# Optimization experiments

Measured on AMD Instinct MI355X. Metric: run time of the kernel, lower is better.

## Reference

```python
import jax, jax.numpy as jnp
import numpy as np
from jax import lax


def _lstm_last(x, Wih, Whh, bih, bhh):
    """Single-layer torch-style LSTM (gate order i,f,g,o); returns last hidden state.
    x: (M, T, F) -> (M, H)."""
    gx = jnp.einsum('mtf,gf->mtg', x, Wih) + bih + bhh  # precompute input contributions
    H = Whh.shape[1]
    Wh = Whh.T
    def step(carry, g):
        h, c = carry
        z = g + h @ Wh
        i, f, gg, o = jnp.split(z, 4, axis=-1)
        c = jax.nn.sigmoid(f) * c + jax.nn.sigmoid(i) * jnp.tanh(gg)
        h = jax.nn.sigmoid(o) * jnp.tanh(c)
        return (h, c), None
    M = x.shape[0]
    init = (jnp.zeros((M, H), x.dtype), jnp.zeros((M, H), x.dtype))
    (h, _), _ = lax.scan(step, init, jnp.swapaxes(gx, 0, 1))
    return h


def _forward(input_data, rel_encoding, lstm_Wih, lstm_Whh, lstm_bih, lstm_bhh,
             hop_w1, hop_b1, hop_w2, hop_b2, fn_w1, fn_b1, fn_w2, fn_b2):
    B, W, N, F = input_data.shape
    U = lstm_Whh.shape[1]
    # SequentialEmbedding: per-stock LSTM over the window, take last step
    x = jnp.transpose(input_data, (0, 2, 1, 3)).reshape(B * N, W, F)
    seq = _lstm_last(x, lstm_Wih, lstm_Whh, lstm_bih, lstm_bhh).reshape(B, N, U)

    # RelationalEmbedding: dense N x N k-hop message passing
    mask = (rel_encoding.sum(-1) > 0).astype(seq.dtype)  # (N,N)
    D = mask.sum(-1)                                      # (N,) degrees (self-loops keep >0)
    e = seq
    for k in range(hop_w1.shape[0]):  # k_hops: small fixed loop
        W1 = hop_w1[k]
        # mask * concat([e_i, e_j, enc]) @ W1 + b1, computed blockwise without
        # materializing the (B,N,N,2U+K) concat; mask scales only the pre-bias term
        xi = e @ W1[:U]                                    # (B,N,INP)
        xj = e @ W1[U:2 * U]                               # (B,N,INP)
        xe = jnp.einsum('ijk,kp->ijp', rel_encoding, W1[2 * U:])  # (N,N,INP)
        pre = mask[None, :, :, None] * (xi[:, :, None, :] + xj[:, None, :, :] + xe[None]) + hop_b1[k]
        hdn = jax.nn.leaky_relu(pre)                       # (B,N,N,INP)
        wts = jax.nn.leaky_relu(hdn @ hop_w2[k] + hop_b2[k])[..., 0]  # (B,N,N)
        scaled = (wts * mask) / D[None, :, None]
        # torch: sum_i scaled[b,i,j] * e_j  ==  e_j * (sum_i scaled[b,i,j])
        e = scaled.sum(axis=1)[..., None] * e

    # FullyConnected head: Linear(2U,2U)+LeakyReLU, Linear(2U,1)+LeakyReLU, squeeze
    comb = jnp.concatenate([seq, e], axis=-1)              # (B,N,2U)
    out = jax.nn.leaky_relu(comb @ fn_w1 + fn_b1)
    out = jax.nn.leaky_relu(out @ fn_w2 + fn_b2)
    return out[..., 0]                                     # (B,N)


def setup_inputs() -> dict:
    key = jax.random.key(0)
    ks = jax.random.split(key, 14)
    B, W, N, F = 2, 32, 768, 4
    U, K, KH = 32, 8, 2
    INP = 2 * U + K  # 72
    def w(k, shape, fan):
        return jax.random.normal(k, shape, jnp.float32) / np.float32(np.sqrt(fan))
    enc = (jax.random.uniform(ks[1], (N, N, K)) < 0.05).astype(jnp.float32)
    # self-loops in relation channel 0 so every node has degree >= 1
    enc = enc.at[:, :, 0].set(jnp.maximum(enc[:, :, 0], jnp.eye(N, dtype=jnp.float32)))
    return {
        'input_data': jax.random.normal(ks[0], (B, W, N, F), jnp.float32),
        'rel_encoding': enc,
        'lstm_Wih': w(ks[2], (4 * U, F), F),
        'lstm_Whh': w(ks[3], (4 * U, U), U),
        'lstm_bih': 0.01 * jax.random.normal(ks[4], (4 * U,), jnp.float32),
        'lstm_bhh': 0.01 * jax.random.normal(ks[5], (4 * U,), jnp.float32),
        'hop_w1': w(ks[6], (KH, INP, INP), INP),
        'hop_b1': 0.01 * jax.random.normal(ks[7], (KH, INP), jnp.float32),
        'hop_w2': w(ks[8], (KH, INP, 1), INP),
        'hop_b2': 0.01 * jax.random.normal(ks[9], (KH, 1), jnp.float32),
        'fn_w1': w(ks[10], (2 * U, 2 * U), 2 * U),
        'fn_b1': 0.01 * jax.random.normal(ks[11], (2 * U,), jnp.float32),
        'fn_w2': w(ks[12], (2 * U, 1), 2 * U),
        'fn_b2': 0.01 * jax.random.normal(ks[13], (1,), jnp.float32),
    }


def reference(input_data, rel_encoding, lstm_Wih, lstm_Whh, lstm_bih, lstm_bhh,
              hop_w1, hop_b1, hop_w2, hop_b2, fn_w1, fn_b1, fn_w2, fn_b2):
    return _forward(input_data, rel_encoding, lstm_Wih, lstm_Whh, lstm_bih, lstm_bhh,
                    hop_w1, hop_b1, hop_w2, hop_b2, fn_w1, fn_b1, fn_w2, fn_b2)
```

## Files before the change

kernel.cpp:

```cpp
#include <hip/hip_runtime.h>

#define N_STK 768
#define BATCH 2
#define WIN   32
#define FEAT  4
#define UNITS 32
#define INP   72
#define LROW  76
#define NSLC  19
#define IPH   48
#define JCR   24
#define NPHI  16
#define NCR   32

__device__ __forceinline__ float lrelu(float v){ return v > 0.0f ? v : 0.01f*v; }
__device__ __forceinline__ float lanebcast(float v, int l){
    return __int_as_float(__builtin_amdgcn_readlane(__float_as_int(v), l));
}
__device__ __forceinline__ unsigned patof(const float* __restrict__ p){
    float4 a = *reinterpret_cast<const float4*>(p);
    float4 b = *reinterpret_cast<const float4*>(p + 4);
    unsigned m = 0;
    m |= (a.x != 0.0f) ? 1u   : 0u;
    m |= (a.y != 0.0f) ? 2u   : 0u;
    m |= (a.z != 0.0f) ? 4u   : 0u;
    m |= (a.w != 0.0f) ? 8u   : 0u;
    m |= (b.x != 0.0f) ? 16u  : 0u;
    m |= (b.y != 0.0f) ? 32u  : 0u;
    m |= (b.z != 0.0f) ? 64u  : 0u;
    m |= (b.w != 0.0f) ? 128u : 0u;
    return m;
}
__device__ __forceinline__ void async_cp16(const float* g, float* l){
    __builtin_amdgcn_global_load_lds(
        (const __attribute__((address_space(1))) unsigned int*)g,
        (__attribute__((address_space(3))) unsigned int*)l,
        16, 0, 0);
}

__global__ __launch_bounds__(256) void k1_kernel(const float* __restrict__ rel,
        const float* __restrict__ x, const float* __restrict__ Wih,
        const float* __restrict__ Whh, const float* __restrict__ bih,
        const float* __restrict__ bhh, const float* __restrict__ hop_w1,
        const float* __restrict__ hop_b1,
        float* __restrict__ seq, float* __restrict__ invD,
        unsigned char* __restrict__ Pout,
        float* __restrict__ lutlo, float* __restrict__ luthi,
        float* __restrict__ xi0, float* __restrict__ xj0,
        float* __restrict__ s0, float* __restrict__ s1){
    int j = blockIdx.x, tid = threadIdx.x;
    int wv = tid >> 6, lane = tid & 63;
    __shared__ float hrow[2][UNITS];
    __shared__ int cw_sh[2];

    if (wv < 2){
        int b = wv;
        int r0 = lane, r1 = 64 + lane;
        bool low = (lane < 32);
        float4 wi0 = *reinterpret_cast<const float4*>(Wih + r0*FEAT);
        float4 wi1 = *reinterpret_cast<const float4*>(Wih + r1*FEAT);
        float bb0 = bih[r0] + bhh[r0];
        float bb1 = bih[r1] + bhh[r1];
        float4 W0[8], W1[8];
        #pragma unroll
        for (int q = 0; q < 8; q++){
            W0[q] = *reinterpret_cast<const float4*>(Whh + r0*UNITS + q*4);
            W1[q] = *reinterpret_cast<const float4*>(Whh + r1*UNITS + q*4);
        }
        float4 xv = make_float4(0.f, 0.f, 0.f, 0.f);
        if (low) xv = *reinterpret_cast<const float4*>(x + ((size_t)(b*WIN + lane)*N_STK + j)*FEAT);
        float hreg = 0.0f, c = 0.0f;
        #pragma unroll 1
        for (int t = 0; t < WIN; t++){
            float xb0 = lanebcast(xv.x, t), xb1 = lanebcast(xv.y, t);
            float xb2 = lanebcast(xv.z, t), xb3 = lanebcast(xv.w, t);
            float z0a = bb0 + wi0.x*xb0 + wi0.z*xb2;
            float z0b =       wi0.y*xb1 + wi0.w*xb3;
            float z1a = bb1 + wi1.x*xb0 + wi1.z*xb2;
            float z1b =       wi1.y*xb1 + wi1.w*xb3;
            #pragma unroll
            for (int q = 0; q < 8; q++){
                float h0 = lanebcast(hreg, 32 + q*4 + 0);
                float h1 = lanebcast(hreg, 32 + q*4 + 1);
                float h2 = lanebcast(hreg, 32 + q*4 + 2);
                float h3 = lanebcast(hreg, 32 + q*4 + 3);
                z0a += W0[q].x*h0; z0b += W0[q].y*h1;
                z0a += W0[q].z*h2; z0b += W0[q].w*h3;
                z1a += W1[q].x*h0; z1b += W1[q].y*h1;
                z1a += W1[q].z*h2; z1b += W1[q].w*h3;
            }
            float z0 = z0a + z0b, z1 = z1a + z1b;
            float e0 = __expf(-z0);
            float sg = 1.0f/(1.0f + e0);
            float sc = low ? -2.0f : -1.0f;
            float e1 = __expf(sc*z1);
            float rr = 1.0f/(1.0f + e1);
            float act = low ? (1.0f - e1)*rr : rr;
            float pa = sg*act;
            float po = __shfl_xor(pa, 32);
            c = sg*c + po;
            float e2 = __expf(-2.0f*c);
            float th = (1.0f - e2)/(1.0f + e2);
            hreg = act*th;
        }
        if (!low){
            hrow[b][lane - 32] = hreg;
            seq[((size_t)b*N_STK + j)*UNITS + (lane - 32)] = hreg;
        }
    } else {
        int half = wv - 2;
        int local = 0;
        #pragma unroll
        for (int k = 0; k < 6; k++){
            int col = half*384 + k*64 + lane;
            unsigned pt = patof(rel + ((size_t)j*N_STK + col)*8);
            Pout[(size_t)j*N_STK + col] = (unsigned char)pt;
            local += pt ? 1 : 0;
        }
        #pragma unroll
        for (int d = 32; d; d >>= 1) local += __shfl_xor(local, d);
        if (lane == 0) cw_sh[half] = local;
    }
    __syncthreads();
    if (tid == 0){
        invD[j] = 1.0f/(float)(cw_sh[0] + cw_sh[1]);
        s0[j] = 0.0f; s0[N_STK + j] = 0.0f;
        s1[j] = 0.0f; s1[N_STK + j] = 0.0f;
    }
    if (j < 64 && tid >= 144 && tid < 216){
        int pp = tid - 144;
        int m = j & 15, half = (j >> 4) & 1, k = j >> 5;
        const float* W = hop_w1 + (size_t)k*INP*INP;
        float acc = half ? 0.0f : hop_b1[k*INP + pp];
        int base = 2*UNITS + (half ? 4 : 0);
        #pragma unroll
        for (int q = 0; q < 4; q++)
            if ((m >> q) & 1) acc += W[(base + q)*INP + pp];
        (half ? luthi : lutlo)[(k*16 + m)*INP + pp] = acc;
    }
    if (tid < 2*INP){
        int b = tid/INP, pp = tid - b*INP;
        float si = 0.0f, sj = 0.0f;
        #pragma unroll
        for (int u = 0; u < UNITS; u++){
            float ev = hrow[b][u];
            si += ev * hop_w1[u*INP + pp];
            sj += ev * hop_w1[(UNITS + u)*INP + pp];
        }
        size_t o = ((size_t)b*N_STK + j)*INP + pp;
        xi0[o] = si; xj0[o] = sj;
    }
}

__global__ __launch_bounds__(256) void hop_kernel(const float* __restrict__ xi,
        const float* __restrict__ xj,
        const float* __restrict__ lutlo_k, const float* __restrict__ luthi_k,
        const float* __restrict__ w2, const float* __restrict__ b2,
        const unsigned char* __restrict__ P, const float* __restrict__ invD,
        float* __restrict__ s_out){
    int cr = blockIdx.x, ip = blockIdx.y, b = blockIdx.z;
    int j0 = cr*JCR, i0 = ip*IPH, tid = threadIdx.x;
    __shared__ float xi_sh[IPH*LROW];
    __shared__ float xj_sh[JCR*LROW];
    __shared__ float lo_sh[16*LROW];
    __shared__ float hi_sh[16*LROW];
    __shared__ float invD_sh[IPH];
    __shared__ float acc_sh[JCR];
    __shared__ unsigned elist[IPH*JCR];
    __shared__ int n0_sh, nt_sh;

    const float* xib = xi + ((size_t)b*N_STK + i0)*INP;
    const float* xjb = xj + ((size_t)b*N_STK + j0)*INP;
    if (tid >= 224 && tid < 224 + JCR) acc_sh[tid - 224] = 0.0f;

    for (int u = tid; u < IPH*NSLC; u += 256){
        int r = u/NSLC, sl = u - r*NSLC;
        int off = (sl < 18) ? sl*4 : 0;
        async_cp16(xib + (size_t)r*INP + off, &xi_sh[0] + (size_t)u*4);
    }
    for (int u = tid; u < JCR*NSLC; u += 256){
        int r = u/NSLC, sl = u - r*NSLC;
        int off = (sl < 18) ? sl*4 : 0;
        async_cp16(xjb + (size_t)r*INP + off, &xj_sh[0] + (size_t)u*4);
    }
    for (int u = tid; u < 16*NSLC; u += 256){
        int r = u/NSLC, sl = u - r*NSLC;
        int off = (sl < 18) ? sl*4 : 0;
        async_cp16(lutlo_k + r*INP + off, &lo_sh[0] + (size_t)u*4);
    }
    for (int u = tid; u < 16*NSLC; u += 256){
        int r = u/NSLC, sl = u - r*NSLC;
        int off = (sl < 18) ? sl*4 : 0;
        async_cp16(luthi_k + r*INP + off, &hi_sh[0] + (size_t)u*4);
    }
    if (tid < IPH/4) async_cp16(invD + i0 + tid*4, &invD_sh[0] + tid*4);

    if (tid < 64){
        unsigned w[6] = {0,0,0,0,0,0};
        int c0 = 0, c1 = 0;
        if (tid < IPH){
            const unsigned* prow = reinterpret_cast<const unsigned*>(P + (size_t)(i0 + tid)*N_STK + j0);
            #pragma unroll
            for (int k = 0; k < 6; k++) w[k] = prow[k];
            #pragma unroll
            for (int k = 0; k < 24; k++){
                unsigned pat = (w[k >> 2] >> ((k & 3)*8)) & 255u;
                c0 += (pat && pat < 16u) ? 1 : 0;
                c1 += (pat >= 16u) ? 1 : 0;
            }
        }
        int s0v = c0, s1v = c1;
        #pragma unroll
        for (int off = 1; off < 64; off <<= 1){
            int a0 = __shfl_up(s0v, off), a1 = __shfl_up(s1v, off);
            if (tid >= off){ s0v += a0; s1v += a1; }
        }
        int N0 = __shfl(s0v, 63);
        int Nt = N0 + __shfl(s1v, 63);
        if (tid < IPH){
            int p0 = s0v - c0, p1 = N0 + s1v - c1;
            #pragma unroll
            for (int k = 0; k < 24; k++){
                unsigned pat = (w[k >> 2] >> ((k & 3)*8)) & 255u;
                unsigned enc = ((unsigned)tid << 13) | ((unsigned)k << 8) | pat;
                if (pat && pat < 16u) elist[p0++] = enc;
                else if (pat >= 16u)  elist[p1++] = enc;
            }
        }
        if (tid == 0){ n0_sh = N0; nt_sh = Nt; }
    }

    int hf = tid & 1;
    float4 w2r[9];
    #pragma unroll
    for (int q = 0; q < 9; q++) w2r[q] = *reinterpret_cast<const float4*>(w2 + hf*36 + q*4);
    float b2v = b2[0];
    __syncthreads();

    int n0 = n0_sh, ntot = nt_sh;
    for (int sl = tid >> 1; sl < n0; sl += 128){
        unsigned ent = elist[sl];
        int il = ent >> 13, jl = (ent >> 8) & 31, mlo = (int)(ent & 15u);
        const float* xr = &xi_sh[il*LROW + hf*36];
        const float* jr = &xj_sh[jl*LROW + hf*36];
        const float* lr = &lo_sh[mlo*LROW + hf*36];
        float dot = 0.0f;
        #pragma unroll
        for (int q = 0; q < 9; q++){
            float4 xv = *reinterpret_cast<const float4*>(xr + q*4);
            float4 jv = *reinterpret_cast<const float4*>(jr + q*4);
            float4 lv = *reinterpret_cast<const float4*>(lr + q*4);
            float4 w  = w2r[q];
            dot += lrelu(xv.x + jv.x + lv.x)*w.x;
            dot += lrelu(xv.y + jv.y + lv.y)*w.y;
            dot += lrelu(xv.z + jv.z + lv.z)*w.z;
            dot += lrelu(xv.w + jv.w + lv.w)*w.w;
        }
        dot += __shfl_xor(dot, 1);
        if (hf == 0) atomicAdd(&acc_sh[jl], lrelu(dot + b2v)*invD_sh[il]);
    }
    for (int sl = n0 + (tid >> 1); sl < ntot; sl += 128){
        unsigned ent = elist[sl];
        int il = ent >> 13, jl = (ent >> 8) & 31;
        int mlo = (int)(ent & 15u), mhi = (int)((ent >> 4) & 15u);
        const float* xr = &xi_sh[il*LROW + hf*36];
        const float* jr = &xj_sh[jl*LROW + hf*36];
        const float* lr = &lo_sh[mlo*LROW + hf*36];
        const float* hr = &hi_sh[mhi*LROW + hf*36];
        float dot = 0.0f;
        #pragma unroll
        for (int q = 0; q < 9; q++){
            float4 xv = *reinterpret_cast<const float4*>(xr + q*4);
            float4 jv = *reinterpret_cast<const float4*>(jr + q*4);
            float4 lv = *reinterpret_cast<const float4*>(lr + q*4);
            float4 hv = *reinterpret_cast<const float4*>(hr + q*4);
            float4 w  = w2r[q];
            dot += lrelu(xv.x + jv.x + lv.x + hv.x)*w.x;
            dot += lrelu(xv.y + jv.y + lv.y + hv.y)*w.y;
            dot += lrelu(xv.z + jv.z + lv.z + hv.z)*w.z;
            dot += lrelu(xv.w + jv.w + lv.w + hv.w)*w.w;
        }
        dot += __shfl_xor(dot, 1);
        if (hf == 0) atomicAdd(&acc_sh[jl], lrelu(dot + b2v)*invD_sh[il]);
    }
    __syncthreads();
    if (tid < JCR) atomicAdd(&s_out[b*N_STK + j0 + tid], acc_sh[tid]);
}

template<int MODE>
__global__ __launch_bounds__(192) void ep_kernel(const float* __restrict__ s0v,
        const float* __restrict__ s1v, const float* __restrict__ seqg,
        const float* __restrict__ W1next, float* __restrict__ xi_next,
        float* __restrict__ xj_next,
        const float* __restrict__ fw1, const float* __restrict__ fb1,
        const float* __restrict__ fw2, const float* __restrict__ fb2,
        float* __restrict__ outp){
    int j = blockIdx.x, tid = threadIdx.x;
    __shared__ float e_sh[2][64];
    if (tid < 64){
        int b = tid >> 5, u = tid & 31;
        size_t o = ((size_t)b*N_STK + j)*UNITS + u;
        float sv = seqg[o];
        if (MODE == 0){
            e_sh[b][u] = sv*s0v[b*N_STK + j];
        } else {
            e_sh[b][u] = sv;
            e_sh[b][32 + u] = sv*s0v[b*N_STK + j]*s1v[b*N_STK + j];
        }
    }
    __syncthreads();
    if (MODE == 0){
        if (tid < 2*INP){
            int b = tid/INP, pp = tid - b*INP;
            float si = 0.0f, sj = 0.0f;
            #pragma unroll
            for (int u = 0; u < UNITS; u++){
                float ev = e_sh[b][u];
                si += ev * W1next[u*INP + pp];
                sj += ev * W1next[(UNITS + u)*INP + pp];
            }
            size_t o = ((size_t)b*N_STK + j)*INP + pp;
            xi_next[o] = si; xj_next[o] = sj;
        }
    } else {
        if (tid < 128){
            int b = tid >> 6, u = tid & 63;
            float acc = fb1[u];
            #pragma unroll 8
            for (int d = 0; d < 64; d++) acc += e_sh[b][d]*fw1[d*64 + u];
            float prod = lrelu(acc)*fw2[u];
            prod += __shfl_xor(prod, 32);
            prod += __shfl_xor(prod, 16);
            prod += __shfl_xor(prod, 8);
            prod += __shfl_xor(prod, 4);
            prod += __shfl_xor(prod, 2);
            prod += __shfl_xor(prod, 1);
            if (u == 0) outp[b*N_STK + j] = lrelu(prod + fb2[0]);
        }
    }
}

extern "C" void kernel_launch(void* const* d_in, const int* in_sizes, int n_in,
                              void* d_out, int out_size, void* d_ws, size_t ws_size,
                              hipStream_t stream){
    const float* input_data = (const float*)d_in[0];
    const float* rel        = (const float*)d_in[1];
    const float* lstm_Wih   = (const float*)d_in[2];
    const float* lstm_Whh   = (const float*)d_in[3];
    const float* lstm_bih   = (const float*)d_in[4];
    const float* lstm_bhh   = (const float*)d_in[5];
    const float* hop_w1     = (const float*)d_in[6];
    const float* hop_b1     = (const float*)d_in[7];
    const float* hop_w2     = (const float*)d_in[8];
    const float* hop_b2     = (const float*)d_in[9];
    const float* fn_w1      = (const float*)d_in[10];
    const float* fn_b1      = (const float*)d_in[11];
    const float* fn_w2      = (const float*)d_in[12];
    const float* fn_b2      = (const float*)d_in[13];
    float* out = (float*)d_out;

    float* ws    = (float*)d_ws;
    float* seq   = ws;
    float* xi0   = seq   + 49152;
    float* xj0   = xi0   + 110592;
    float* xi1   = xj0   + 110592;
    float* xj1   = xi1   + 110592;
    float* lutlo = xj1   + 110592;
    float* luthi = lutlo + 2304;
    float* invD  = luthi + 2304;
    float* s0    = invD  + 768;
    float* s1    = s0    + 1536;
    unsigned char* P = (unsigned char*)(s1 + 1536);

    k1_kernel<<<N_STK, 256, 0, stream>>>(rel, input_data, lstm_Wih, lstm_Whh,
            lstm_bih, lstm_bhh, hop_w1, hop_b1,
            seq, invD, P, lutlo, luthi, xi0, xj0, s0, s1);

    dim3 hgrid(NCR, NPHI, BATCH);
    hop_kernel<<<hgrid, 256, 0, stream>>>(xi0, xj0, lutlo, luthi,
            hop_w2, hop_b2, P, invD, s0);

    ep_kernel<0><<<N_STK, 192, 0, stream>>>(s0, nullptr, seq,
            hop_w1 + INP*INP, xi1, xj1,
            nullptr, nullptr, nullptr, nullptr, nullptr);

    hop_kernel<<<hgrid, 256, 0, stream>>>(xi1, xj1, lutlo + 16*INP, luthi + 16*INP,
            hop_w2 + INP, hop_b2 + 1, P, invD, s1);

    ep_kernel<1><<<N_STK, 192, 0, stream>>>(s0, s1, seq,
            nullptr, nullptr, nullptr,
            fn_w1, fn_b1, fn_w2, fn_b2, out);
}
```

Measured before the change: 149.1 us.

## Precompute second-hop projections in LSTM kernel and scale by s0 inside hop kernel

Because e after the first hop equals seq scaled by a per-node scalar, the second hop's xi/xj projections are linear in that scalar. k1 now also computes seq@W1[hop1] projections, and the second hop kernel multiplies them by s0[i] and s0[j] on the fly. This removes the intermediate ep_kernel launch and its global round-trip. The cost is extra multiplies in the hop inner loop and more work in k1.

```diff
diff --git a/kernel.cpp b/kernel.cpp
--- a/kernel.cpp
+++ b/kernel.cpp
@@ -47,6 +47,7 @@
         unsigned char* __restrict__ Pout,
         float* __restrict__ lutlo, float* __restrict__ luthi,
         float* __restrict__ xi0, float* __restrict__ xj0,
+        float* __restrict__ yi1, float* __restrict__ yj1,
         float* __restrict__ s0, float* __restrict__ s1){
     int j = blockIdx.x, tid = threadIdx.x;
     int wv = tid >> 6, lane = tid & 63;
@@ -140,24 +141,30 @@
     }
     if (tid < 2*INP){
         int b = tid/INP, pp = tid - b*INP;
-        float si = 0.0f, sj = 0.0f;
+        const float* Wa = hop_w1;
+        const float* Wb = hop_w1 + INP*INP;
+        float si0 = 0.0f, sj0 = 0.0f, si1 = 0.0f, sj1 = 0.0f;
         #pragma unroll
         for (int u = 0; u < UNITS; u++){
             float ev = hrow[b][u];
-            si += ev * hop_w1[u*INP + pp];
-            sj += ev * hop_w1[(UNITS + u)*INP + pp];
+            si0 += ev * Wa[u*INP + pp];
+            sj0 += ev * Wa[(UNITS + u)*INP + pp];
+            si1 += ev * Wb[u*INP + pp];
+            sj1 += ev * Wb[(UNITS + u)*INP + pp];
         }
         size_t o = ((size_t)b*N_STK + j)*INP + pp;
-        xi0[o] = si; xj0[o] = sj;
-    }
-}
-
+        xi0[o] = si0; xj0[o] = sj0;
+        yi1[o] = si1; yj1[o] = sj1;
+    }
+}
+
+template<int SCALED>
 __global__ __launch_bounds__(256) void hop_kernel(const float* __restrict__ xi,
         const float* __restrict__ xj,
         const float* __restrict__ lutlo_k, const float* __restrict__ luthi_k,
         const float* __restrict__ w2, const float* __restrict__ b2,
         const unsigned char* __restrict__ P, const float* __restrict__ invD,
-        float* __restrict__ s_out){
+        const float* __restrict__ sscale, float* __restrict__ s_out){
     int cr = blockIdx.x, ip = blockIdx.y, b = blockIdx.z;
     int j0 = cr*JCR, i0 = ip*IPH, tid = threadIdx.x;
     __shared__ float xi_sh[IPH*LROW];
@@ -165,6 +172,8 @@
     __shared__ float lo_sh[16*LROW];
     __shared__ float hi_sh[16*LROW];
     __shared__ float invD_sh[IPH];
+    __shared__ float sI_sh[IPH];
+    __shared__ float sJ_sh[JCR];
     __shared__ float acc_sh[JCR];
     __shared__ unsigned elist[IPH*JCR];
     __shared__ int n0_sh, nt_sh;
@@ -172,6 +181,11 @@
     const float* xib = xi + ((size_t)b*N_STK + i0)*INP;
     const float* xjb = xj + ((size_t)b*N_STK + j0)*INP;
     if (tid >= 224 && tid < 224 + JCR) acc_sh[tid - 224] = 0.0f;
+
+    if (SCALED){
+        if (tid >= 160 && tid < 160 + IPH) sI_sh[tid - 160] = sscale[b*N_STK + i0 + (tid - 160)];
+        if (tid >= 128 && tid < 128 + JCR) sJ_sh[tid - 128] = sscale[b*N_STK + j0 + (tid - 128)];
+    }
 
     for (int u = tid; u < IPH*NSLC; u += 256){
         int r = u/NSLC, sl = u - r*NSLC;
@@ -244,6 +258,8 @@
         const float* xr = &xi_sh[il*LROW + hf*36];
         const float* jr = &xj_sh[jl*LROW + hf*36];
         const float* lr = &lo_sh[mlo*LROW + hf*36];
+        float si = SCALED ? sI_sh[il] : 1.0f;
+        float sj = SCALED ? sJ_sh[jl] : 1.0f;
         float dot = 0.0f;
         #pragma unroll
         for (int q = 0; q < 9; q++){
@@ -251,10 +267,17 @@
             float4 jv = *reinterpret_cast<const float4*>(jr + q*4);
             float4 lv = *reinterpret_cast<const float4*>(lr + q*4);
             float4 w  = w2r[q];
-            dot += lrelu(xv.x + jv.x + lv.x)*w.x;
-            dot += lrelu(xv.y + jv.y + lv.y)*w.y;
-            dot += lrelu(xv.z + jv.z + lv.z)*w.z;
-            dot += lrelu(xv.w + jv.w + lv.w)*w.w;
+            if (SCALED){
+                dot += lrelu(si*xv.x + sj*jv.x + lv.x)*w.x;
+                dot += lrelu(si*xv.y + sj*jv.y + lv.y)*w.y;
+                dot += lrelu(si*xv.z + sj*jv.z + lv.z)*w.z;
+                dot += lrelu(si*xv.w + sj*jv.w + lv.w)*w.w;
+            } else {
+                dot += lrelu(xv.x + jv.x + lv.x)*w.x;
+                dot += lrelu(xv.y + jv.y + lv.y)*w.y;
+                dot += lrelu(xv.z + jv.z + lv.z)*w.z;
+                dot += lrelu(xv.w + jv.w + lv.w)*w.w;
+            }
         }
         dot += __shfl_xor(dot, 1);
         if (hf == 0) atomicAdd(&acc_sh[jl], lrelu(dot + b2v)*invD_sh[il]);
@@ -267,6 +290,8 @@
         const float* jr = &xj_sh[jl*LROW + hf*36];
         const float* lr = &lo_sh[mlo*LROW + hf*36];
         const float* hr = &hi_sh[mhi*LROW + hf*36];
+        float si = SCALED ? sI_sh[il] : 1.0f;
+        float sj = SCALED ? sJ_sh[jl] : 1.0f;
         float dot = 0.0f;
         #pragma unroll
         for (int q = 0; q < 9; q++){
@@ -275,10 +300,17 @@
             float4 lv = *reinterpret_cast<const float4*>(lr + q*4);
             float4 hv = *reinterpret_cast<const float4*>(hr + q*4);
             float4 w  = w2r[q];
-            dot += lrelu(xv.x + jv.x + lv.x + hv.x)*w.x;
-            dot += lrelu(xv.y + jv.y + lv.y + hv.y)*w.y;
-            dot += lrelu(xv.z + jv.z + lv.z + hv.z)*w.z;
-            dot += lrelu(xv.w + jv.w + lv.w + hv.w)*w.w;
+            if (SCALED){
+                dot += lrelu(si*xv.x + sj*jv.x + lv.x + hv.x)*w.x;
+                dot += lrelu(si*xv.y + sj*jv.y + lv.y + hv.y)*w.y;
+                dot += lrelu(si*xv.z + sj*jv.z + lv.z + hv.z)*w.z;
+                dot += lrelu(si*xv.w + sj*jv.w + lv.w + hv.w)*w.w;
+            } else {
+                dot += lrelu(xv.x + jv.x + lv.x + hv.x)*w.x;
+                dot += lrelu(xv.y + jv.y + lv.y + hv.y)*w.y;
+                dot += lrelu(xv.z + jv.z + lv.z + hv.z)*w.z;
+                dot += lrelu(xv.w + jv.w + lv.w + hv.w)*w.w;
+            }
         }
         dot += __shfl_xor(dot, 1);
         if (hf == 0) atomicAdd(&acc_sh[jl], lrelu(dot + b2v)*invD_sh[il]);
@@ -287,11 +319,8 @@
     if (tid < JCR) atomicAdd(&s_out[b*N_STK + j0 + tid], acc_sh[tid]);
 }
 
-template<int MODE>
-__global__ __launch_bounds__(192) void ep_kernel(const float* __restrict__ s0v,
+__global__ __launch_bounds__(128) void head_kernel(const float* __restrict__ s0v,
         const float* __restrict__ s1v, const float* __restrict__ seqg,
-        const float* __restrict__ W1next, float* __restrict__ xi_next,
-        float* __restrict__ xj_next,
         const float* __restrict__ fw1, const float* __restrict__ fb1,
         const float* __restrict__ fw2, const float* __restrict__ fb2,
         float* __restrict__ outp){
@@ -301,43 +330,22 @@
         int b = tid >> 5, u = tid & 31;
         size_t o = ((size_t)b*N_STK + j)*UNITS + u;
         float sv = seqg[o];
-        if (MODE == 0){
-            e_sh[b][u] = sv*s0v[b*N_STK + j];
-        } else {
-            e_sh[b][u] = sv;
-            e_sh[b][32 + u] = sv*s0v[b*N_STK + j]*s1v[b*N_STK + j];
-        }
+        e_sh[b][u] = sv;
+        e_sh[b][32 + u] = sv*s0v[b*N_STK + j]*s1v[b*N_STK + j];
     }
     __syncthreads();
-    if (MODE == 0){
-        if (tid < 2*INP){
-            int b = tid/INP, pp = tid - b*INP;
-            float si = 0.0f, sj = 0.0f;
-            #pragma unroll
-            for (int u = 0; u < UNITS; u++){
-                float ev = e_sh[b][u];
-                si += ev * W1next[u*INP + pp];
-                sj += ev * W1next[(UNITS + u)*INP + pp];
-            }
-            size_t o = ((size_t)b*N_STK + j)*INP + pp;
-            xi_next[o] = si; xj_next[o] = sj;
-        }
-    } else {
-        if (tid < 128){
-            int b = tid >> 6, u = tid & 63;
-            float acc = fb1[u];
-            #pragma unroll 8
-            for (int d = 0; d < 64; d++) acc += e_sh[b][d]*fw1[d*64 + u];
-            float prod = lrelu(acc)*fw2[u];
-            prod += __shfl_xor(prod, 32);
-            prod += __shfl_xor(prod, 16);
-            prod += __shfl_xor(prod, 8);
-            prod += __shfl_xor(prod, 4);
-            prod += __shfl_xor(prod, 2);
-            prod += __shfl_xor(prod, 1);
-            if (u == 0) outp[b*N_STK + j] = lrelu(prod + fb2[0]);
-        }
-    }
+    int b = tid >> 6, u = tid & 63;
+    float acc = fb1[u];
+    #pragma unroll 8
+    for (int d = 0; d < 64; d++) acc += e_sh[b][d]*fw1[d*64 + u];
+    float prod = lrelu(acc)*fw2[u];
+    prod += __shfl_xor(prod, 32);
+    prod += __shfl_xor(prod, 16);
+    prod += __shfl_xor(prod, 8);
+    prod += __shfl_xor(prod, 4);
+    prod += __shfl_xor(prod, 2);
+    prod += __shfl_xor(prod, 1);
+    if (u == 0) outp[b*N_STK + j] = lrelu(prod + fb2[0]);
 }
 
 extern "C" void kernel_launch(void* const* d_in, const int* in_sizes, int n_in,
@@ -363,9 +371,9 @@
     float* seq   = ws;
     float* xi0   = seq   + 49152;
     float* xj0   = xi0   + 110592;
-    float* xi1   = xj0   + 110592;
-    float* xj1   = xi1   + 110592;
-    float* lutlo = xj1   + 110592;
+    float* yi1   = xj0   + 110592;
+    float* yj1   = yi1   + 110592;
+    float* lutlo = yj1   + 110592;
     float* luthi = lutlo + 2304;
     float* invD  = luthi + 2304;
     float* s0    = invD  + 768;
@@ -374,20 +382,15 @@
 
     k1_kernel<<<N_STK, 256, 0, stream>>>(rel, input_data, lstm_Wih, lstm_Whh,
             lstm_bih, lstm_bhh, hop_w1, hop_b1,
-            seq, invD, P, lutlo, luthi, xi0, xj0, s0, s1);
+            seq, invD, P, lutlo, luthi, xi0, xj0, yi1, yj1, s0, s1);
 
     dim3 hgrid(NCR, NPHI, BATCH);
-    hop_kernel<<<hgrid, 256, 0, stream>>>(xi0, xj0, lutlo, luthi,
-            hop_w2, hop_b2, P, invD, s0);
-
-    ep_kernel<0><<<N_STK, 192, 0, stream>>>(s0, nullptr, seq,
-            hop_w1 + INP*INP, xi1, xj1,
-            nullptr, nullptr, nullptr, nullptr, nullptr);
-
-    hop_kernel<<<hgrid, 256, 0, stream>>>(xi1, xj1, lutlo + 16*INP, luthi + 16*INP,
-            hop_w2 + INP, hop_b2 + 1, P, invD, s1);
-
-    ep_kernel<1><<<N_STK, 192, 0, stream>>>(s0, s1, seq,
-            nullptr, nullptr, nullptr,
+    hop_kernel<0><<<hgrid, 256, 0, stream>>>(xi0, xj0, lutlo, luthi,
+            hop_w2, hop_b2, P, invD, nullptr, s0);
+
+    hop_kernel<1><<<hgrid, 256, 0, stream>>>(yi1, yj1, lutlo + 16*INP, luthi + 16*INP,
+            hop_w2 + INP, hop_b2 + 1, P, invD, s0, s1);
+
+    head_kernel<<<N_STK, 128, 0, stream>>>(s0, s1, seq,
             fn_w1, fn_b1, fn_w2, fn_b2, out);
 }
```

After: 155.4 us. 1.04x slower.
